# Performance work log

Hardware: AMD Instinct MI355X
Metric: run time of the kernel (lower is better)

Reference implementation:

```python
import jax, jax.numpy as jnp
import numpy as np

EPS = 1e-5

def bn(x, gamma, beta, axes):
    # training-mode batchnorm over `axes`, channel axis = 1 (matches nn.BatchNorm1d/2d)
    mean = jnp.mean(x, axis=axes, keepdims=True)
    var = jnp.var(x, axis=axes, keepdims=True)
    shp = [1] * x.ndim
    shp[1] = -1
    return gamma.reshape(shp) * (x - mean) * jax.lax.rsqrt(var + EPS) + beta.reshape(shp)

def setup_inputs():
    key = jax.random.key(0)
    B, N, K, Cin, Cout, m = 4, 4096, 32, 64, 64, 8
    ks = jax.random.split(key, 10)
    def w(k, shape, fan_in):
        return jax.random.normal(k, shape, jnp.float32) * np.float32(np.sqrt(2.0 / fan_in))
    return {
        "x": jax.random.normal(ks[0], (B, Cin, N), jnp.float32),
        "xyz_score": jax.random.normal(ks[1], (B, 66, N, K), jnp.float32),
        "conv1_w": w(ks[2], (Cin, Cin), Cin),
        "bn1_g": jnp.ones((Cin,), jnp.float32), "bn1_b": jnp.zeros((Cin,), jnp.float32),
        "matrice2": w(ks[3], (Cin, m * Cout), Cin),  # weight bank: i x (m*o)
        "sn_w0": w(ks[4], (64, 66), 66), "sn_g0": jnp.ones((64,), jnp.float32), "sn_b0": jnp.zeros((64,), jnp.float32),
        "sn_w1": w(ks[5], (32, 64), 64), "sn_g1": jnp.ones((32,), jnp.float32), "sn_b1": jnp.zeros((32,), jnp.float32),
        "sn_w2": w(ks[6], (16, 32), 32), "sn_g2": jnp.ones((16,), jnp.float32), "sn_b2": jnp.zeros((16,), jnp.float32),
        "sn_w3": w(ks[7], (m, 16), 16), "sn_bias3": jnp.zeros((m,), jnp.float32),
        "bn2_g": jnp.ones((Cout,), jnp.float32), "bn2_b": jnp.zeros((Cout,), jnp.float32),
        "idx": jax.random.randint(ks[8], (B, N, K), 0, N, dtype=jnp.int32),
    }

def reference(x, xyz_score, conv1_w, bn1_g, bn1_b, matrice2,
              sn_w0, sn_g0, sn_b0, sn_w1, sn_g1, sn_b1, sn_w2, sn_g2, sn_b2,
              sn_w3, sn_bias3, bn2_g, bn2_b, idx):
    B, Cin, N = x.shape
    m = sn_w3.shape[0]
    # conv1 (1x1, no bias) + BN1 + ReLU  -> [B, Cin, N]
    h = jnp.einsum('oc,bcn->bon', conv1_w, x)
    h = jax.nn.relu(bn(h, bn1_g, bn1_b, (0, 2)))
    # feat_trans_pointnet: [B,N,Cin] @ [Cin, m*Cout] -> [B,N,m,Cout]
    y = jnp.einsum('bcn,ck->bnk', h, matrice2).reshape(B, N, m, -1)
    # ScoreNet: stack of 1x1 conv2d + BN + ReLU, final conv with bias, softmax over m
    s = xyz_score  # [B, 66, N, K]
    s = jax.nn.relu(bn(jnp.einsum('oc,bcnk->bonk', sn_w0, s), sn_g0, sn_b0, (0, 2, 3)))
    s = jax.nn.relu(bn(jnp.einsum('oc,bcnk->bonk', sn_w1, s), sn_g1, sn_b1, (0, 2, 3)))
    s = jax.nn.relu(bn(jnp.einsum('oc,bcnk->bonk', sn_w2, s), sn_g2, sn_b2, (0, 2, 3)))
    s = jnp.einsum('oc,bcnk->bonk', sn_w3, s) + sn_bias3[None, :, None, None]
    score = jax.nn.softmax(s, axis=1)            # [B, m, N, K], bias=0
    score = jnp.transpose(score, (0, 2, 3, 1))   # [B, N, K, m]
    # assemble_pointnet: gather neighbor transformed feats and score-weight them
    neigh = y[jnp.arange(B)[:, None, None], idx]             # [B, N, K, m, Cout]
    out = jnp.einsum('bnkm,bnkmo->bon', score, neigh)        # [B, Cout, N]
    return jax.nn.relu(bn(out, bn2_g, bn2_b, (0, 2)))
```

## Files before the change

kernel.cpp:

```cpp
#include <hip/hip_runtime.h>
#include <cstdint>

typedef unsigned short u16;
typedef unsigned int   u32;
typedef __attribute__((ext_vector_type(8))) short short8;
typedef __attribute__((ext_vector_type(4))) float f32x4;

constexpr int CB = 4;
constexpr int CN = 4096;
constexpr int CK = 32;
constexpr int NPTS = CB * CN * CK;
constexpr int NBK  = 131072;
constexpr float EPSV = 1e-5f;

struct __align__(16) Q4 { u32 a, b, c, d; };

static __device__ __forceinline__ u16 f2b(float f) {
  union { float f; u32 u; } v; v.f = f;
  u32 u = v.u;
  return (u16)((u + 0x7FFFu + ((u >> 16) & 1u)) >> 16);
}
static __device__ __forceinline__ float b2f(u16 h) {
  union { u32 u; float f; } v; v.u = ((u32)h) << 16;
  return v.f;
}
static __device__ __forceinline__ u32 pk2(float lo, float hi) {
  return (u32)f2b(lo) | ((u32)f2b(hi) << 16);
}
static __device__ __forceinline__ short8 mk8(u32 a, u32 b, u32 c, u32 d) {
  union { u32 w[4]; short8 v; } u; u.w[0]=a; u.w[1]=b; u.w[2]=c; u.w[3]=d; return u.v;
}

__global__ __launch_bounds__(256) void k_conv1(const float* __restrict__ x,
                                               const float* __restrict__ w,
                                               float* __restrict__ h,
                                               float* S, float* Q) {
  __shared__ float wl[64 * 64];
  __shared__ float ls[128];
  int tid = threadIdx.x;
  for (int i = tid; i < 4096; i += 256) wl[i] = w[i];
  if (tid < 128) ls[tid] = 0.f;
  __syncthreads();
  int col = blockIdx.x * 256 + tid;
  int b = col >> 12, n = col & 4095;
  float xr[64];
  const float* xp = x + (size_t)(b * 64) * CN + n;
  #pragma unroll
  for (int c = 0; c < 64; ++c) xr[c] = xp[(size_t)c * CN];
  int lane = tid & 63;
  for (int o = 0; o < 64; ++o) {
    float acc = 0.f;
    const float* wr = &wl[o * 64];
    #pragma unroll
    for (int c = 0; c < 64; ++c) acc = fmaf(wr[c], xr[c], acc);
    h[(size_t)(b * 64 + o) * CN + n] = acc;
    float v = acc, v2 = acc * acc;
    for (int d = 1; d < 64; d <<= 1) { v += __shfl_xor(v, d); v2 += __shfl_xor(v2, d); }
    if (lane == 0) { atomicAdd(&ls[o], v); atomicAdd(&ls[64 + o], v2); }
  }
  __syncthreads();
  if (tid < 64) atomicAdd(&S[tid], ls[tid]);
  else if (tid < 128) atomicAdd(&Q[tid - 64], ls[tid]);
}

__global__ __launch_bounds__(64) void k_affine(const float* S, const float* Q,
                                               const float* g, const float* bt,
                                               float* A, float* Bo, int C, float inv_cnt) {
  int t = threadIdx.x;
  if (t < C) {
    float mean = S[t] * inv_cnt;
    float var = fmaxf(Q[t] * inv_cnt - mean * mean, 0.f);
    float a = g[t] * rsqrtf(var + EPSV);
    A[t] = a;
    Bo[t] = bt[t] - mean * a;
  }
}

__global__ __launch_bounds__(256) void k_prepM2(const float* __restrict__ M2,
                                                u16* __restrict__ m2frag) {
  int i = blockIdx.x * 256 + threadIdx.x;
  int e = i & 7, lane = (i >> 3) & 63, t = i >> 9;
  int mt = t >> 1, kc = t & 1;
  int row = 16 * mt + (lane & 15);
  int k = 32 * kc + 8 * (lane >> 4) + e;
  m2frag[i] = f2b(M2[k * 512 + row]);
}

__global__ __launch_bounds__(256) void k_y(const float* __restrict__ h,
                                           const u16* __restrict__ m2frag,
                                           const float* __restrict__ Ah,
                                           const float* __restrict__ Bh,
                                           u16* __restrict__ y16) {
  __shared__ u16 yl[4][16 * 520];
  __shared__ float abl[128];
  int tid = threadIdx.x;
  if (tid < 64) abl[tid] = Ah[tid];
  else if (tid < 128) abl[tid] = Bh[tid - 64];
  int wv = tid >> 6, lane = tid & 63, g = lane >> 4, pl = lane & 15;
  __syncthreads();
  int wid = blockIdx.x * 4 + wv;
  int n0 = wid * 16;
  int b = n0 >> 12, nloc = n0 & 4095;
  const float* sb = h + (size_t)(b * 64) * CN + nloc + pl;
  u32 w[8];
  #pragma unroll
  for (int kc = 0; kc < 2; ++kc) {
    #pragma unroll
    for (int e2 = 0; e2 < 4; ++e2) {
      int c0 = 32 * kc + 8 * g + 2 * e2;
      float v0 = fmaxf(fmaf(abl[c0],     sb[(size_t)c0 * CN],       abl[64 + c0]),     0.f);
      float v1 = fmaxf(fmaf(abl[c0 + 1], sb[(size_t)(c0 + 1) * CN], abl[64 + c0 + 1]), 0.f);
      w[kc * 4 + e2] = pk2(v0, v1);
    }
  }
  short8 Bf0 = mk8(w[0], w[1], w[2], w[3]);
  short8 Bf1 = mk8(w[4], w[5], w[6], w[7]);
  const short8* m2f = (const short8*)m2frag;
  u16* ylw = &yl[wv][0];
  #pragma unroll
  for (int mt = 0; mt < 32; ++mt) {
    short8 A0 = m2f[(mt * 2 + 0) * 64 + lane];
    short8 A1 = m2f[(mt * 2 + 1) * 64 + lane];
    f32x4 z = {0.f, 0.f, 0.f, 0.f};
    z = __builtin_amdgcn_mfma_f32_16x16x32_bf16(A0, Bf0, z, 0, 0, 0);
    z = __builtin_amdgcn_mfma_f32_16x16x32_bf16(A1, Bf1, z, 0, 0, 0);
    u32* wp = (u32*)&ylw[pl * 520 + 16 * mt + 4 * g];
    wp[0] = pk2(z[0], z[1]);
    wp[1] = pk2(z[2], z[3]);
  }
  u16* yg = y16 + (size_t)n0 * 512;
  for (int j = 0; j < 16; ++j) {
    short8 v = *(const short8*)&ylw[j * 520 + lane * 8];
    *(short8*)(yg + (size_t)j * 512 + lane * 8) = v;
  }
}

static __device__ __forceinline__ void ld_frags(const float* __restrict__ xyz,
                                                int c, int g, int pl, short8 fr[5]) {
  int pbase = c * 32;
  int b = pbase >> 17, r = pbase & (NBK - 1);
  const float* base = xyz + (size_t)b * 66 * NBK + r + g * 8;
  #pragma unroll
  for (int ci = 0; ci < 4; ++ci) {
    const float* p = base + (size_t)(16 * ci + pl) * NBK;
    float4 v0 = *(const float4*)p;
    float4 v1 = *(const float4*)(p + 4);
    fr[ci] = mk8(pk2(v0.x, v0.y), pk2(v0.z, v0.w), pk2(v1.x, v1.y), pk2(v1.z, v1.w));
  }
  if (pl < 2) {
    const float* p = base + (size_t)(64 + pl) * NBK;
    float4 v0 = *(const float4*)p;
    float4 v1 = *(const float4*)(p + 4);
    fr[4] = mk8(pk2(v0.x, v0.y), pk2(v0.z, v0.w), pk2(v1.x, v1.y), pk2(v1.z, v1.w));
  } else if (pl == 2) {
    fr[4] = mk8(0x3F803F80u, 0x3F803F80u, 0x3F803F80u, 0x3F803F80u);
  } else {
    fr[4] = mk8(0u, 0u, 0u, 0u);
  }
}

__global__ __launch_bounds__(256) void k_moment(const float* __restrict__ xyz,
                                                float* __restrict__ Mpart) {
  constexpr int TI[15] = {0,0,0,0,0,1,1,1,1,2,2,2,3,3,4};
  constexpr int TJ[15] = {0,1,2,3,4,1,2,3,4,2,3,4,3,4,4};
  int tid = threadIdx.x;
  int wv = tid >> 6;
  int wid = blockIdx.x * 4 + wv;
  int lane = tid & 63, g = lane >> 4, pl = lane & 15;
  f32x4 acc[15];
  #pragma unroll
  for (int t = 0; t < 15; ++t) acc[t] = (f32x4){0.f, 0.f, 0.f, 0.f};
  for (int cc = wid; cc < NPTS / 32; cc += 4096) {
    short8 fr0[5], fr1[5];
    ld_frags(xyz, cc,        g, pl, fr0);
    ld_frags(xyz, cc + 2048, g, pl, fr1);
    #pragma unroll
    for (int t = 0; t < 15; ++t)
      acc[t] = __builtin_amdgcn_mfma_f32_16x16x32_bf16(fr0[TI[t]], fr0[TJ[t]], acc[t], 0, 0, 0);
    #pragma unroll
    for (int t = 0; t < 15; ++t)
      acc[t] = __builtin_amdgcn_mfma_f32_16x16x32_bf16(fr1[TI[t]], fr1[TJ[t]], acc[t], 0, 0, 0);
  }
  float* mp = Mpart + (size_t)wid * 3840;
  #pragma unroll
  for (int t = 0; t < 15; ++t)
    *(f32x4*)(mp + t * 256 + lane * 4) = acc[t];
}

__global__ __launch_bounds__(256) void k_mreduce(const float* __restrict__ Mpart,
                                                 float* __restrict__ M) {
  int e = blockIdx.x * 256 + threadIdx.x;
  int kg = blockIdx.y;
  float s = 0.f;
  for (int k = kg * 256; k < kg * 256 + 256; ++k) s += Mpart[(size_t)k * 3840 + e];
  atomicAdd(&M[e], s);
}

__global__ __launch_bounds__(256) void k_affine1m(const float* __restrict__ M,
                                                  const float* __restrict__ w0,
                                                  const float* __restrict__ g0,
                                                  const float* __restrict__ b0,
                                                  float* __restrict__ A1,
                                                  float* __restrict__ B1) {
  __shared__ float lsM[67 * 68];
  __shared__ float w0l[64 * 69];
  __shared__ float red[4 * 64];
  int tid = threadIdx.x;
  const float inv = 1.f / (float)NPTS;
  for (int i = tid; i < 67 * 67; i += 256) {
    int r = i / 67, c = i % 67;
    int rr = r, cc = c;
    if ((r >> 4) > (c >> 4)) { rr = c; cc = r; }
    int ti = rr >> 4, tj = cc >> 4;
    int t = ti * (9 - ti) / 2 + tj;
    int rho = rr & 15, kap = cc & 15;
    lsM[r * 68 + c] = M[t * 256 + ((rho >> 2) * 16 + kap) * 4 + (rho & 3)] * inv;
  }
  for (int i = tid; i < 64 * 66; i += 256) {
    int o = i / 66, c = i % 66;
    w0l[o * 69 + c] = w0[i];
  }
  __syncthreads();
  int o = tid & 63, sl = tid >> 6;
  float acc2 = 0.f;
  for (int c1 = sl * 17; c1 < sl * 17 + 17; ++c1) {
    if (c1 >= 66) break;
    float inner = 0.f;
    const float* mr = &lsM[c1 * 68];
    const float* wr = &w0l[o * 69];
    for (int c2 = 0; c2 < 66; ++c2) inner = fmaf(mr[c2], wr[c2], inner);
    acc2 = fmaf(wr[c1], inner, acc2);
  }
  red[sl * 64 + o] = acc2;
  __syncthreads();
  if (sl == 0) {
    float Ez2 = red[o] + red[64 + o] + red[128 + o] + red[192 + o];
    float mean = 0.f;
    const float* wr = &w0l[o * 69];
    for (int c = 0; c < 66; ++c) mean = fmaf(wr[c], lsM[c * 68 + 66], mean);
    float var = fmaxf(Ez2 - mean * mean, 0.f);
    float a = g0[o] * rsqrtf(var + EPSV);
    A1[o] = a;
    B1[o] = b0[o] - mean * a;
  }
}

__global__ __launch_bounds__(256) void k_prep(const float* __restrict__ w0,
                                              const float* __restrict__ w1,
                                              const float* __restrict__ A1,
                                              const float* __restrict__ B1,
                                              u16* __restrict__ w0frag,
                                              u16* __restrict__ w1frag) {
  int tid = threadIdx.x;
  for (int i = tid; i < 6144; i += 256) {
    int e = i & 7, lane = (i >> 3) & 63, t = i >> 9;
    int mt = t / 3, kc = t % 3;
    int row = 16 * mt + (lane & 15);
    int k = 32 * kc + 8 * (lane >> 4) + e;
    float v;
    if (k < 66)      v = A1[row] * w0[row * 66 + k];
    else if (k == 66) v = B1[row];
    else              v = 0.f;
    w0frag[i] = f2b(v);
  }
  for (int i = tid; i < 2048; i += 256) {
    int e = i & 7, lane = (i >> 3) & 63, t = i >> 9;
    int m2t = t >> 1, kc2 = t & 1;
    int row = 16 * m2t + (lane & 15);
    int k = 32 * kc2 + 8 * (lane >> 4) + e;
    w1frag[i] = f2b(w1[row * 64 + k]);
  }
}

__global__ __launch_bounds__(256) void k_s2(const float* __restrict__ xyz,
                                            const u16* __restrict__ w0frag,
                                            const u16* __restrict__ w1frag,
                                            u32* __restrict__ z2p,
                                            float* S, float* Q) {
  __shared__ u16 a1l[4][16][80];
  __shared__ float ls2[64];
  int tid = threadIdx.x;
  int wv = tid >> 6, lane = tid & 63, g = lane >> 4, pl = lane & 15;
  if (tid < 64) ls2[tid] = 0.f;
  __syncthreads();

  const short8* w0f = (const short8*)w0frag;
  const short8* w1f = (const short8*)w1frag;
  short8 A0[4][3];
  #pragma unroll
  for (int mt = 0; mt < 4; ++mt)
    #pragma unroll
    for (int kc = 0; kc < 3; ++kc) A0[mt][kc] = w0f[(mt * 3 + kc) * 64 + lane];
  short8 W1f[2][2];
  #pragma unroll
  for (int m2t = 0; m2t < 2; ++m2t)
    #pragma unroll
    for (int kc2 = 0; kc2 < 2; ++kc2) W1f[m2t][kc2] = w1f[(m2t * 2 + kc2) * 64 + lane];

  float sum8[8], sq8[8];
  #pragma unroll
  for (int i = 0; i < 8; ++i) { sum8[i] = 0.f; sq8[i] = 0.f; }

  int wid = blockIdx.x * 4 + wv;
  for (int s = wid; s < NPTS / 16; s += 8192) {
    int pg = s * 16;
    int b = pg >> 17, r = pg & (NBK - 1);
    const float* sb = xyz + (size_t)b * 66 * NBK + r + pl;
    float v[16];
    #pragma unroll
    for (int e = 0; e < 8; ++e) v[e]     = sb[(size_t)(8 * g + e) * NBK];
    #pragma unroll
    for (int e = 0; e < 8; ++e) v[8 + e] = sb[(size_t)(32 + 8 * g + e) * NBK];
    u32 c2a = 0u, c2b = 0u;
    if (g == 0) {
      float v64 = sb[(size_t)64 * NBK];
      float v65 = sb[(size_t)65 * NBK];
      c2a = pk2(v64, v65);
      c2b = 0x00003F80u;
    }
    short8 Bf0 = mk8(pk2(v[0], v[1]), pk2(v[2], v[3]), pk2(v[4], v[5]), pk2(v[6], v[7]));
    short8 Bf1 = mk8(pk2(v[8], v[9]), pk2(v[10], v[11]), pk2(v[12], v[13]), pk2(v[14], v[15]));
    short8 Bf2 = mk8(c2a, c2b, 0u, 0u);

    #pragma unroll
    for (int mt = 0; mt < 4; ++mt) {
      f32x4 z = {0.f, 0.f, 0.f, 0.f};
      z = __builtin_amdgcn_mfma_f32_16x16x32_bf16(A0[mt][0], Bf0, z, 0, 0, 0);
      z = __builtin_amdgcn_mfma_f32_16x16x32_bf16(A0[mt][1], Bf1, z, 0, 0, 0);
      z = __builtin_amdgcn_mfma_f32_16x16x32_bf16(A0[mt][2], Bf2, z, 0, 0, 0);
      float r0 = fmaxf(z[0], 0.f), r1 = fmaxf(z[1], 0.f);
      float r2 = fmaxf(z[2], 0.f), r3 = fmaxf(z[3], 0.f);
      u32* wp = (u32*)&a1l[wv][pl][16 * mt + 4 * g];
      wp[0] = pk2(r0, r1);
      wp[1] = pk2(r2, r3);
    }
    short8 B2f0 = *(const short8*)&a1l[wv][pl][8 * g];
    short8 B2f1 = *(const short8*)&a1l[wv][pl][32 + 8 * g];
    #pragma unroll
    for (int m2t = 0; m2t < 2; ++m2t) {
      f32x4 z2 = {0.f, 0.f, 0.f, 0.f};
      z2 = __builtin_amdgcn_mfma_f32_16x16x32_bf16(W1f[m2t][0], B2f0, z2, 0, 0, 0);
      z2 = __builtin_amdgcn_mfma_f32_16x16x32_bf16(W1f[m2t][1], B2f1, z2, 0, 0, 0);
      #pragma unroll
      for (int rr = 0; rr < 4; ++rr) {
        sum8[m2t * 4 + rr] += z2[rr];
        sq8[m2t * 4 + rr] += z2[rr] * z2[rr];
      }
      int jlo = 8 * m2t + 2 * g;
      z2p[(size_t)jlo * NPTS + pg + pl]       = pk2(z2[0], z2[1]);
      z2p[(size_t)(jlo + 1) * NPTS + pg + pl] = pk2(z2[2], z2[3]);
    }
  }
  #pragma unroll
  for (int i = 0; i < 8; ++i) {
    float vS = sum8[i], vQ = sq8[i];
    for (int d = 1; d < 16; d <<= 1) { vS += __shfl_xor(vS, d); vQ += __shfl_xor(vQ, d); }
    if (pl == 0) {
      int ch = 16 * (i >> 2) + 4 * g + (i & 3);
      atomicAdd(&ls2[ch], vS);
      atomicAdd(&ls2[32 + ch], vQ);
    }
  }
  __syncthreads();
  if (tid < 32) atomicAdd(&S[tid], ls2[tid]);
  else if (tid < 64) atomicAdd(&Q[tid - 32], ls2[tid]);
}

__global__ __launch_bounds__(256) void k_s3(const u32* __restrict__ z2p,
                                            const float* __restrict__ w2,
                                            const float* __restrict__ A2,
                                            const float* __restrict__ B2,
                                            u32* __restrict__ z3,
                                            float* S, float* Q) {
  __shared__ float w2l[16 * 32];
  __shared__ float ab[64];
  __shared__ float ls[32];
  int tid = threadIdx.x;
  for (int i = tid; i < 512; i += 256) w2l[i] = w2[i];
  if (tid < 32) { ab[tid] = A2[tid]; ls[tid] = 0.f; }
  else if (tid < 64) ab[tid] = B2[tid - 32];
  __syncthreads();
  int p = blockIdx.x * 256 + tid;
  float a2[32];
  #pragma unroll
  for (int j = 0; j < 16; ++j) {
    u32 wj = z2p[(size_t)j * NPTS + p];
    float lo = b2f((u16)(wj & 0xFFFFu));
    float hi = b2f((u16)(wj >> 16));
    a2[2 * j]     = fmaxf(fmaf(ab[2 * j], lo, ab[32 + 2 * j]), 0.f);
    a2[2 * j + 1] = fmaxf(fmaf(ab[2 * j + 1], hi, ab[32 + 2 * j + 1]), 0.f);
  }
  int lane = tid & 63;
  float zt[16];
  for (int j = 0; j < 16; ++j) {
    float z = 0.f;
    const float* wr = &w2l[j * 32];
    #pragma unroll
    for (int c = 0; c < 32; ++c) z = fmaf(wr[c], a2[c], z);
    zt[j] = z;
    float v = z, v2 = z * z;
    for (int d = 1; d < 64; d <<= 1) { v += __shfl_xor(v, d); v2 += __shfl_xor(v2, d); }
    if (lane == 0) { atomicAdd(&ls[j], v); atomicAdd(&ls[16 + j], v2); }
  }
  u32 pkk[8];
  #pragma unroll
  for (int j = 0; j < 8; ++j) pkk[j] = pk2(zt[2 * j], zt[2 * j + 1]);
  Q4* dst = (Q4*)(z3 + (size_t)p * 8);
  #pragma unroll
  for (int i = 0; i < 2; ++i) { Q4 q; q.a = pkk[4*i]; q.b = pkk[4*i+1]; q.c = pkk[4*i+2]; q.d = pkk[4*i+3]; dst[i] = q; }
  __syncthreads();
  if (tid < 16) atomicAdd(&S[tid], ls[tid]);
  else if (tid < 32) atomicAdd(&Q[tid - 16], ls[tid]);
}

__global__ __launch_bounds__(256) void k_score(const u32* __restrict__ z3,
                                               const float* __restrict__ w3,
                                               const float* __restrict__ bias3,
                                               const float* __restrict__ A3,
                                               const float* __restrict__ B3,
                                               float* __restrict__ scores) {
  __shared__ float w3l[128];
  __shared__ float bl[8];
  __shared__ float ab[32];
  int tid = threadIdx.x;
  if (tid < 128) w3l[tid] = w3[tid];
  if (tid < 8) bl[tid] = bias3[tid];
  if (tid < 16) ab[tid] = A3[tid];
  else if (tid < 32) ab[tid] = B3[tid - 16];
  __syncthreads();
  int p = blockIdx.x * 256 + tid;
  const Q4* zp = (const Q4*)(z3 + (size_t)p * 8);
  Q4 r0 = zp[0], r1 = zp[1];
  u32 w8[8] = {r0.a, r0.b, r0.c, r0.d, r1.a, r1.b, r1.c, r1.d};
  float a3[16];
  #pragma unroll
  for (int t = 0; t < 8; ++t) {
    int c = t * 2;
    a3[c]     = fmaxf(fmaf(ab[c], b2f((u16)(w8[t] & 0xFFFFu)), ab[16 + c]), 0.f);
    a3[c + 1] = fmaxf(fmaf(ab[c + 1], b2f((u16)(w8[t] >> 16)), ab[16 + c + 1]), 0.f);
  }
  float z4[8]; float mx = -1e30f;
  #pragma unroll
  for (int mI = 0; mI < 8; ++mI) {
    float z = bl[mI];
    const float* wr = &w3l[mI * 16];
    #pragma unroll
    for (int c = 0; c < 16; ++c) z = fmaf(wr[c], a3[c], z);
    z4[mI] = z; mx = fmaxf(mx, z);
  }
  float ssum = 0.f;
  #pragma unroll
  for (int mI = 0; mI < 8; ++mI) { z4[mI] = __expf(z4[mI] - mx); ssum += z4[mI]; }
  float inv = 1.f / ssum;
  float4* sp = (float4*)(scores + (size_t)p * 8);
  sp[0] = make_float4(z4[0] * inv, z4[1] * inv, z4[2] * inv, z4[3] * inv);
  sp[1] = make_float4(z4[4] * inv, z4[5] * inv, z4[6] * inv, z4[7] * inv);
}

__global__ __launch_bounds__(256) void k_gather(const u16* __restrict__ y16,
                                                const float* __restrict__ scores,
                                                const int* __restrict__ idx,
                                                float* __restrict__ out0,
                                                float* S, float* Q) {
  __shared__ float ls[128];
  int tid = threadIdx.x;
  if (tid < 128) ls[tid] = 0.f;
  __syncthreads();
  int bid = blockIdx.x;
  int batch = (bid & 7) >> 1;
  int sub = ((bid >> 3) << 1) | (bid & 1);
  int wv = tid >> 6, lane = tid & 63;
  int m = lane >> 3, og = lane & 7;
  const u16* ybase = y16 + (size_t)batch * CN * 512;
  for (int i = 0; i < 2; ++i) {
    int pid = (batch << 12) + sub * 8 + wv * 2 + i;
    int pbase = pid * 32;
    float acc8[8] = {0, 0, 0, 0, 0, 0, 0, 0};
    for (int k = 0; k < 32; ++k) {
      int p = pbase + k;
      int j = idx[p];
      float s = scores[(size_t)p * 8 + m];
      short8 yv = *(const short8*)(ybase + ((size_t)j << 9) + lane * 8);
      #pragma unroll
      for (int t = 0; t < 8; ++t)
        acc8[t] = fmaf(s, b2f((u16)yv[t]), acc8[t]);
    }
    #pragma unroll
    for (int d = 8; d < 64; d <<= 1) {
      #pragma unroll
      for (int t = 0; t < 8; ++t) acc8[t] += __shfl_xor(acc8[t], d);
    }
    if (m == 0) {
      float* op = out0 + (size_t)pid * 64 + og * 8;
      *(float4*)op       = make_float4(acc8[0], acc8[1], acc8[2], acc8[3]);
      *(float4*)(op + 4) = make_float4(acc8[4], acc8[5], acc8[6], acc8[7]);
      #pragma unroll
      for (int t = 0; t < 8; ++t) {
        atomicAdd(&ls[og * 8 + t], acc8[t]);
        atomicAdd(&ls[64 + og * 8 + t], acc8[t] * acc8[t]);
      }
    }
  }
  __syncthreads();
  if (tid < 64) atomicAdd(&S[tid], ls[tid]);
  else if (tid < 128) atomicAdd(&Q[tid - 64], ls[tid]);
}

__global__ __launch_bounds__(256) void k_bn2(const float* __restrict__ out0,
                                             const float* __restrict__ A,
                                             const float* __restrict__ Bo,
                                             float* __restrict__ outp) {
  int gid = blockIdx.x * 256 + threadIdx.x;
  for (int i = gid; i < CB * 64 * CN; i += 262144) {
    int b = i >> 18, o = (i >> 12) & 63, n = i & 4095;
    float v = out0[((size_t)((b << 12) | n)) * 64 + o];
    outp[i] = fmaxf(fmaf(A[o], v, Bo[o]), 0.f);
  }
}

extern "C" void kernel_launch(void* const* d_in, const int* in_sizes, int n_in,
                              void* d_out, int out_size, void* d_ws, size_t ws_size,
                              hipStream_t stream) {
  const float* x       = (const float*)d_in[0];
  const float* xyz     = (const float*)d_in[1];
  const float* conv1_w = (const float*)d_in[2];
  const float* bn1_g   = (const float*)d_in[3];
  const float* bn1_b   = (const float*)d_in[4];
  const float* M2      = (const float*)d_in[5];
  const float* w0      = (const float*)d_in[6];
  const float* g0      = (const float*)d_in[7];
  const float* b0      = (const float*)d_in[8];
  const float* w1      = (const float*)d_in[9];
  const float* g1      = (const float*)d_in[10];
  const float* b1      = (const float*)d_in[11];
  const float* w2      = (const float*)d_in[12];
  const float* g2      = (const float*)d_in[13];
  const float* b2      = (const float*)d_in[14];
  const float* w3      = (const float*)d_in[15];
  const float* bias3   = (const float*)d_in[16];
  const float* bn2_g   = (const float*)d_in[17];
  const float* bn2_b   = (const float*)d_in[18];
  const int*   idx     = (const int*)d_in[19];
  float* out = (float*)d_out;

  char* wsb = (char*)d_ws;
  float* h      = (float*)wsb;
  u16*   y16    = (u16*)(wsb + 4194304);
  float* scores = (float*)(wsb + 20971520);
  u32*   z2p    = (u32*)(wsb + 37748736);
  u32*   z3     = (u32*)(wsb + 71303168);
  float* out0   = (float*)(wsb + 88080384);
  float* sums   = (float*)(wsb + 92274688);
  float* S_h = sums;        float* Q_h = sums + 64;
  float* S_2 = sums + 128;  float* Q_2 = sums + 160;
  float* S_3 = sums + 192;  float* Q_3 = sums + 208;
  float* S_o = sums + 224;  float* Q_o = sums + 288;
  float* Mm  = sums + 352;
  float* A_h = sums + 6752; float* B_h = sums + 6816;
  float* A_1 = sums + 6880; float* B_1 = sums + 6944;
  float* A_2 = sums + 7008; float* B_2 = sums + 7040;
  float* A_3 = sums + 7072; float* B_3 = sums + 7088;
  float* A_o = sums + 7104; float* B_o = sums + 7168;
  u16* w0frag = (u16*)(sums + 7232);
  u16* w1frag = w0frag + 6144;
  u16* m2frag = w1frag + 2048;
  float* Mpart = (float*)z2p;

  hipMemsetAsync(sums, 0, 6752 * sizeof(float), stream);

  k_prepM2<<<128, 256, 0, stream>>>(M2, m2frag);
  k_conv1<<<64, 256, 0, stream>>>(x, conv1_w, h, S_h, Q_h);
  k_affine<<<1, 64, 0, stream>>>(S_h, Q_h, bn1_g, bn1_b, A_h, B_h, 64, 1.f / 16384.f);
  k_y<<<256, 256, 0, stream>>>(h, m2frag, A_h, B_h, y16);

  k_moment<<<512, 256, 0, stream>>>(xyz, Mpart);
  k_mreduce<<<dim3(15, 8), 256, 0, stream>>>(Mpart, Mm);
  k_affine1m<<<1, 256, 0, stream>>>(Mm, w0, g0, b0, A_1, B_1);
  k_prep<<<1, 256, 0, stream>>>(w0, w1, A_1, B_1, w0frag, w1frag);
  k_s2<<<2048, 256, 0, stream>>>(xyz, w0frag, w1frag, z2p, S_2, Q_2);
  k_affine<<<1, 64, 0, stream>>>(S_2, Q_2, g1, b1, A_2, B_2, 32, 1.f / (float)NPTS);
  k_s3<<<2048, 256, 0, stream>>>(z2p, w2, A_2, B_2, z3, S_3, Q_3);
  k_affine<<<1, 64, 0, stream>>>(S_3, Q_3, g2, b2, A_3, B_3, 16, 1.f / (float)NPTS);

  k_score<<<2048, 256, 0, stream>>>(z3, w3, bias3, A_3, B_3, scores);
  k_gather<<<2048, 256, 0, stream>>>(y16, scores, idx, out0, S_o, Q_o);
  k_affine<<<1, 64, 0, stream>>>(S_o, Q_o, bn2_g, bn2_b, A_o, B_o, 64, 1.f / 16384.f);
  k_bn2<<<1024, 256, 0, stream>>>(out0, A_o, B_o, out);
}
```

Baseline: 345.1 us.

## Split conv1 over output-channel groups and interleave two points in gather

k_conv1 now launches four times as many blocks, each computing 16 output channels for 256 columns, so far more of the GPU is busy instead of only 64 blocks. Each block redundantly reloads the 64 input channels it needs. In k_gather, each wave loads all 64 neighbour indices once with one coalesced read and broadcasts them with shuffles. It then processes its two points in one unrolled loop, giving more independent gathers in flight. The cost is more registers per thread, which may lower occupancy.

```diff
diff --git a/kernel.cpp b/kernel.cpp
--- a/kernel.cpp
+++ b/kernel.cpp
@@ -35,32 +35,35 @@
                                                const float* __restrict__ w,
                                                float* __restrict__ h,
                                                float* S, float* Q) {
-  __shared__ float wl[64 * 64];
-  __shared__ float ls[128];
-  int tid = threadIdx.x;
-  for (int i = tid; i < 4096; i += 256) wl[i] = w[i];
-  if (tid < 128) ls[tid] = 0.f;
-  __syncthreads();
-  int col = blockIdx.x * 256 + tid;
+  __shared__ float wl[16 * 64];
+  __shared__ float ls[32];
+  int tid = threadIdx.x;
+  int og = blockIdx.x >> 6;
+  int cb = blockIdx.x & 63;
+  for (int i = tid; i < 1024; i += 256) wl[i] = w[og * 1024 + i];
+  if (tid < 32) ls[tid] = 0.f;
+  __syncthreads();
+  int col = cb * 256 + tid;
   int b = col >> 12, n = col & 4095;
   float xr[64];
   const float* xp = x + (size_t)(b * 64) * CN + n;
   #pragma unroll
   for (int c = 0; c < 64; ++c) xr[c] = xp[(size_t)c * CN];
   int lane = tid & 63;
-  for (int o = 0; o < 64; ++o) {
+  for (int oo = 0; oo < 16; ++oo) {
+    int o = og * 16 + oo;
     float acc = 0.f;
-    const float* wr = &wl[o * 64];
+    const float* wr = &wl[oo * 64];
     #pragma unroll
     for (int c = 0; c < 64; ++c) acc = fmaf(wr[c], xr[c], acc);
     h[(size_t)(b * 64 + o) * CN + n] = acc;
     float v = acc, v2 = acc * acc;
     for (int d = 1; d < 64; d <<= 1) { v += __shfl_xor(v, d); v2 += __shfl_xor(v2, d); }
-    if (lane == 0) { atomicAdd(&ls[o], v); atomicAdd(&ls[64 + o], v2); }
-  }
-  __syncthreads();
-  if (tid < 64) atomicAdd(&S[tid], ls[tid]);
-  else if (tid < 128) atomicAdd(&Q[tid - 64], ls[tid]);
+    if (lane == 0) { atomicAdd(&ls[oo], v); atomicAdd(&ls[16 + oo], v2); }
+  }
+  __syncthreads();
+  if (tid < 16) atomicAdd(&S[og * 16 + tid], ls[tid]);
+  else if (tid < 32) atomicAdd(&Q[og * 16 + tid - 16], ls[tid]);
 }
 
 __global__ __launch_bounds__(64) void k_affine(const float* S, const float* Q,
@@ -472,33 +475,46 @@
   int wv = tid >> 6, lane = tid & 63;
   int m = lane >> 3, og = lane & 7;
   const u16* ybase = y16 + (size_t)batch * CN * 512;
-  for (int i = 0; i < 2; ++i) {
-    int pid = (batch << 12) + sub * 8 + wv * 2 + i;
-    int pbase = pid * 32;
-    float acc8[8] = {0, 0, 0, 0, 0, 0, 0, 0};
-    for (int k = 0; k < 32; ++k) {
-      int p = pbase + k;
-      int j = idx[p];
-      float s = scores[(size_t)p * 8 + m];
-      short8 yv = *(const short8*)(ybase + ((size_t)j << 9) + lane * 8);
-      #pragma unroll
-      for (int t = 0; t < 8; ++t)
-        acc8[t] = fmaf(s, b2f((u16)yv[t]), acc8[t]);
-    }
-    #pragma unroll
-    for (int d = 8; d < 64; d <<= 1) {
-      #pragma unroll
-      for (int t = 0; t < 8; ++t) acc8[t] += __shfl_xor(acc8[t], d);
-    }
-    if (m == 0) {
-      float* op = out0 + (size_t)pid * 64 + og * 8;
-      *(float4*)op       = make_float4(acc8[0], acc8[1], acc8[2], acc8[3]);
-      *(float4*)(op + 4) = make_float4(acc8[4], acc8[5], acc8[6], acc8[7]);
-      #pragma unroll
-      for (int t = 0; t < 8; ++t) {
-        atomicAdd(&ls[og * 8 + t], acc8[t]);
-        atomicAdd(&ls[64 + og * 8 + t], acc8[t] * acc8[t]);
-      }
+  int pid0 = (batch << 12) + sub * 8 + wv * 2;
+  int pbase = pid0 * 32;
+  int jv = idx[pbase + lane];
+  float acc0[8] = {0, 0, 0, 0, 0, 0, 0, 0};
+  float acc1[8] = {0, 0, 0, 0, 0, 0, 0, 0};
+  #pragma unroll 4
+  for (int k = 0; k < 32; ++k) {
+    int j0 = __shfl(jv, k);
+    int j1 = __shfl(jv, 32 + k);
+    float s0 = scores[(size_t)(pbase + k) * 8 + m];
+    float s1 = scores[(size_t)(pbase + 32 + k) * 8 + m];
+    short8 y0 = *(const short8*)(ybase + ((size_t)j0 << 9) + lane * 8);
+    short8 y1 = *(const short8*)(ybase + ((size_t)j1 << 9) + lane * 8);
+    #pragma unroll
+    for (int t = 0; t < 8; ++t) {
+      acc0[t] = fmaf(s0, b2f((u16)y0[t]), acc0[t]);
+      acc1[t] = fmaf(s1, b2f((u16)y1[t]), acc1[t]);
+    }
+  }
+  #pragma unroll
+  for (int d = 8; d < 64; d <<= 1) {
+    #pragma unroll
+    for (int t = 0; t < 8; ++t) {
+      acc0[t] += __shfl_xor(acc0[t], d);
+      acc1[t] += __shfl_xor(acc1[t], d);
+    }
+  }
+  if (m == 0) {
+    float* op0 = out0 + (size_t)pid0 * 64 + og * 8;
+    *(float4*)op0       = make_float4(acc0[0], acc0[1], acc0[2], acc0[3]);
+    *(float4*)(op0 + 4) = make_float4(acc0[4], acc0[5], acc0[6], acc0[7]);
+    float* op1 = out0 + (size_t)(pid0 + 1) * 64 + og * 8;
+    *(float4*)op1       = make_float4(acc1[0], acc1[1], acc1[2], acc1[3]);
+    *(float4*)(op1 + 4) = make_float4(acc1[4], acc1[5], acc1[6], acc1[7]);
+    #pragma unroll
+    for (int t = 0; t < 8; ++t) {
+      float sv = acc0[t] + acc1[t];
+      float qv = acc0[t] * acc0[t] + acc1[t] * acc1[t];
+      atomicAdd(&ls[og * 8 + t], sv);
+      atomicAdd(&ls[64 + og * 8 + t], qv);
     }
   }
   __syncthreads();
@@ -569,7 +585,7 @@
   hipMemsetAsync(sums, 0, 6752 * sizeof(float), stream);
 
   k_prepM2<<<128, 256, 0, stream>>>(M2, m2frag);
-  k_conv1<<<64, 256, 0, stream>>>(x, conv1_w, h, S_h, Q_h);
+  k_conv1<<<256, 256, 0, stream>>>(x, conv1_w, h, S_h, Q_h);
   k_affine<<<1, 64, 0, stream>>>(S_h, Q_h, bn1_g, bn1_b, A_h, B_h, 64, 1.f / 16384.f);
   k_y<<<256, 256, 0, stream>>>(h, m2frag, A_h, B_h, y16);
 
```

New measurement: 312.1 us. -9.6%, faster.
